# Performance work log

Measured on AMD Instinct MI355X. Metric: run time of the kernel, lower is better.

The kernel has to match this reference:

```python
import jax, jax.numpy as jnp
import numpy as np

HEADS = 8
DIM_HEAD = 64
SCALE = DIM_HEAD ** -0.5


def setup_inputs() -> dict:
    key = jax.random.key(0)
    ks = jax.random.split(key, 7)
    B, Nq, Nc = 4, 2048, 2048
    Dq, Dc = 1024, 768
    inner = HEADS * DIM_HEAD  # 512
    x = jax.random.normal(ks[0], (B, Nq, Dq), dtype=jnp.float32)
    context = jax.random.normal(ks[1], (B, Nc, Dc), dtype=jnp.float32)
    # Linear weights stored as (in, out) so y = x @ W, matching torch Linear math.
    Wq = jax.random.normal(ks[2], (Dq, inner), dtype=jnp.float32) * (Dq ** -0.5)
    Wk = jax.random.normal(ks[3], (Dc, inner), dtype=jnp.float32) * (Dc ** -0.5)
    Wv = jax.random.normal(ks[4], (Dc, inner), dtype=jnp.float32) * (Dc ** -0.5)
    Wo = jax.random.normal(ks[5], (inner, Dq), dtype=jnp.float32) * (inner ** -0.5)
    bo = jax.random.normal(ks[6], (Dq,), dtype=jnp.float32) * 0.01
    return {"x": x, "context": context, "Wq": Wq, "Wk": Wk, "Wv": Wv, "Wo": Wo, "bo": bo}


def reference(x, context, Wq, Wk, Wv, Wo, bo):
    B, Nq, _ = x.shape
    # projections -> [b, n, h, d]
    q = (x @ Wq).reshape(B, Nq, HEADS, DIM_HEAD)
    k = (context @ Wk).reshape(B, context.shape[1], HEADS, DIM_HEAD)
    v = (context @ Wv).reshape(B, context.shape[1], HEADS, DIM_HEAD)
    # scores [b, h, i, j]
    sim = jnp.einsum('bihd,bjhd->bhij', q, k) * SCALE
    attn = jax.nn.softmax(sim, axis=-1)
    out = jnp.einsum('bhij,bjhd->bihd', attn, v)  # [b, i, h, d]
    out = out.reshape(B, Nq, HEADS * DIM_HEAD)
    return out @ Wo + bo
```

## Files before the change

### kernel.cpp

```cpp
#include <hip/hip_runtime.h>
#include <hip/hip_bf16.h>


typedef __bf16 bf16_8 __attribute__((ext_vector_type(8)));
typedef __bf16 bf16_4 __attribute__((ext_vector_type(4)));
typedef float f32_4 __attribute__((ext_vector_type(4)));

#define AS1 __attribute__((address_space(1)))
#define AS3 __attribute__((address_space(3)))

__device__ __forceinline__ void gld_lds16(const __bf16* g, __bf16* l) {
  __builtin_amdgcn_global_load_lds((AS1 unsigned int*)(void*)g,
                                   (AS3 unsigned int*)(void*)l, 16, 0, 0);
}

__device__ __forceinline__ void lds_fence() {
  __asm__ volatile("" ::: "memory");
  __builtin_amdgcn_s_waitcnt(0xC07F);
  __asm__ volatile("" ::: "memory");
}

__global__ __launch_bounds__(256) void prep(
    const float* __restrict__ x, const float* __restrict__ ctx,
    const float* __restrict__ Wq, const float* __restrict__ Wk,
    const float* __restrict__ Wv, const float* __restrict__ Wo,
    __bf16* __restrict__ xb, __bf16* __restrict__ ctxb,
    __bf16* __restrict__ WqT, __bf16* __restrict__ WkT,
    __bf16* __restrict__ WvT, __bf16* __restrict__ WoT) {
  int tb = blockIdx.x;
  if (tb >= 1792) {
    tb -= 1792;
    const float* src;
    __bf16* dst;
    size_t base;
    if (tb < 4096) { src = x; dst = xb; base = (size_t)tb * 2048; }
    else { src = ctx; dst = ctxb; base = (size_t)(tb - 4096) * 2048; }
    const size_t idx = base + threadIdx.x * 8;
    const f32_4 f0 = *(const f32_4*)(src + idx);
    const f32_4 f1 = *(const f32_4*)(src + idx + 4);
    bf16_8 v;
#pragma unroll
    for (int i = 0; i < 4; ++i) { v[i] = (__bf16)f0[i]; v[4 + i] = (__bf16)f1[i]; }
    *(bf16_8*)(dst + idx) = v;
    return;
  }
  __shared__ __bf16 t[32][33];
  const float* W; __bf16* Wt; int K, N;
  if (tb < 512)       { W = Wq; Wt = WqT; K = 1024; N = 512; }
  else if (tb < 896)  { tb -= 512;  W = Wk; Wt = WkT; K = 768; N = 512; }
  else if (tb < 1280) { tb -= 896;  W = Wv; Wt = WvT; K = 768; N = 512; }
  else                { tb -= 1280; W = Wo; Wt = WoT; K = 512; N = 1024; }
  const int nx = N >> 5;
  const int n0 = (tb % nx) * 32, k0 = (tb / nx) * 32;
  const int tx = threadIdx.x & 31, ty = threadIdx.x >> 5;
#pragma unroll
  for (int r = 0; r < 32; r += 8)
    t[ty + r][tx] = (__bf16)W[(size_t)(k0 + ty + r) * N + n0 + tx];
  __syncthreads();
#pragma unroll
  for (int r = 0; r < 32; r += 8)
    Wt[(size_t)(n0 + ty + r) * K + k0 + tx] = t[tx][ty + r];
}

__global__ __launch_bounds__(256, 2) void proj(
    const __bf16* __restrict__ xb, const __bf16* __restrict__ ctxb,
    const __bf16* __restrict__ WqT, const __bf16* __restrict__ WkvT,
    __bf16* __restrict__ Qb, __bf16* __restrict__ Kbuf,
    __bf16* __restrict__ Vtb) {
  __shared__ __align__(16) __bf16 As[2][128 * 64];
  __shared__ __align__(16) __bf16 Bs[2][128 * 64];
  int tb = blockIdx.x;
  const __bf16 *A, *Bt;
  int K, bm, bn, mode;
  if (tb < 256) {
    A = xb; Bt = WqT; K = 1024; mode = 0;
    bn = (tb & 3) << 7; bm = (tb >> 2) << 7;
  } else {
    tb -= 256;
    A = ctxb; Bt = WkvT; K = 768; mode = 1;
    bn = (tb & 7) << 7; bm = (tb >> 3) << 7;
  }
  const int tid = threadIdx.x;
  const int lane = tid & 63;
  const int wave = tid >> 6;
  const int wi = (wave >> 1) * 64;
  const int wn = (wave & 1) * 64;
  const int lrow = lane & 15;
  const int quad = lane >> 4;
  const int lkey = lrow & 7;
  const int srow = tid >> 3;
  const int scol = (tid & 7) * 8;
  const int swz = (((scol >> 3) ^ (srow & 7)) * 8);

  f32_4 acc[4][4];
#pragma unroll
  for (int i = 0; i < 4; ++i)
#pragma unroll
    for (int j = 0; j < 4; ++j)
#pragma unroll
      for (int r = 0; r < 4; ++r) acc[i][j][r] = 0.0f;

  auto stage = [&](int buf, int kt) {
#pragma unroll
    for (int r = 0; r < 4; ++r) {
      const int row = r * 32 + srow;
      gld_lds16(A + (size_t)(bm + row) * K + kt + swz, &As[buf][row * 64 + scol]);
    }
#pragma unroll
    for (int r = 0; r < 4; ++r) {
      const int row = r * 32 + srow;
      gld_lds16(Bt + (size_t)(bn + row) * K + kt + swz, &Bs[buf][row * 64 + scol]);
    }
  };

  stage(0, 0);
  const int nkt = K >> 6;
  for (int kti = 0; kti < nkt; ++kti) {
    __syncthreads();
    if (kti + 1 < nkt) stage((kti + 1) & 1, (kti + 1) * 64);
    const __bf16* Asb = As[kti & 1];
    const __bf16* Bsb = Bs[kti & 1];
#pragma unroll
    for (int ks = 0; ks < 2; ++ks) {
      bf16_8 af[4], bfv[4];
#pragma unroll
      for (int t = 0; t < 4; ++t)
        af[t] = *(const bf16_8*)(Asb + (wi + t * 16 + lrow) * 64 +
                                 (((ks * 4 + quad) ^ lkey) * 8));
#pragma unroll
      for (int t = 0; t < 4; ++t)
        bfv[t] = *(const bf16_8*)(Bsb + (wn + t * 16 + lrow) * 64 +
                                  (((ks * 4 + quad) ^ lkey) * 8));
#pragma unroll
      for (int it = 0; it < 4; ++it)
#pragma unroll
        for (int nt = 0; nt < 4; ++nt)
          acc[it][nt] = __builtin_amdgcn_mfma_f32_16x16x32_bf16(
              af[it], bfv[nt], acc[it][nt], 0, 0, 0);
    }
  }

#pragma unroll
  for (int nt = 0; nt < 4; ++nt) {
    const int c = bn + wn + nt * 16 + lrow;
    if (mode == 0) {
#pragma unroll
      for (int it = 0; it < 4; ++it) {
        const int rbase = bm + wi + it * 16 + quad * 4;
#pragma unroll
        for (int r = 0; r < 4; ++r)
          Qb[(size_t)(rbase + r) * 512 + c] = (__bf16)(acc[it][nt][r] * 0.125f);
      }
    } else if (c < 512) {
#pragma unroll
      for (int it = 0; it < 4; ++it) {
        const int rbase = bm + wi + it * 16 + quad * 4;
#pragma unroll
        for (int r = 0; r < 4; ++r)
          Kbuf[(size_t)(rbase + r) * 512 + c] = (__bf16)acc[it][nt][r];
      }
    } else {
      const int vcol = c - 512;
      const int bhh = ((bm >> 11) << 3) + (vcol >> 6);
      const int d = vcol & 63;
#pragma unroll
      for (int it = 0; it < 4; ++it) {
        const int jb = (bm & 2047) + wi + it * 16 + quad * 4;
        bf16_4 pk;
#pragma unroll
        for (int r = 0; r < 4; ++r) pk[r] = (__bf16)acc[it][nt][r];
        *(bf16_4*)&Vtb[((size_t)(bhh * 64 + d)) * 2048 + jb] = pk;
      }
    }
  }
}

__global__ __launch_bounds__(256, 4) void attn_fwd(const __bf16* __restrict__ Q,
                                                   const __bf16* __restrict__ Kb,
                                                   const __bf16* __restrict__ Vt,
                                                   __bf16* __restrict__ AO) {
  __shared__ __align__(16) __bf16 Ks[2][64 * 64];
  __shared__ __align__(16) __bf16 Vs[2][64 * 64];
  __shared__ __align__(16) __bf16 Pl[4][16 * 64];
  const int tid = threadIdx.x;
  const int lane = tid & 63;
  const int wave = tid >> 6;
  const int did = blockIdx.x;
  const int sid = did >> 3;
  const int bh = ((did & 7) << 2) + (sid & 3);
  const int ib = sid >> 2;
  const int b = bh >> 3, h = bh & 7;
  const int i0 = ib * 64 + wave * 16;
  const int lrow = lane & 15;
  const int quad = lane >> 4;
  const int lkey = lrow & 7;
  const size_t bq = (size_t)b * 2048;
  const int hc = h * 64;
  __bf16* Pw = &Pl[wave][0];

  const int ssub = lane >> 3;
  const int sch = lane & 7;
  const int sswz = (sch ^ ssub) * 8;

  const __bf16* Kg = Kb + bq * 512 + hc;
  const __bf16* Vg = Vt + (size_t)bh * 64 * 2048;

  auto stage = [&](int buf, int j0) {
#pragma unroll
    for (int t = 0; t < 2; ++t) {
      const int rb = wave * 16 + t * 8;
      gld_lds16(Kg + (size_t)(j0 + rb + ssub) * 512 + sswz, &Ks[buf][rb * 64]);
      gld_lds16(Vg + (size_t)(rb + ssub) * 2048 + j0 + sswz, &Vs[buf][rb * 64]);
    }
  };

  bf16_8 aq[2];
#pragma unroll
  for (int ks = 0; ks < 2; ++ks)
    aq[ks] = *(const bf16_8*)(Q + (bq + i0 + lrow) * 512 +
                              hc + ks * 32 + quad * 8);

  float psl = 0.0f;
  f32_4 oacc[4];
#pragma unroll
  for (int nt = 0; nt < 4; ++nt)
#pragma unroll
    for (int r = 0; r < 4; ++r) oacc[nt][r] = 0.0f;

  stage(0, 0);

  for (int jt = 0; jt < 32; ++jt) {
    __syncthreads();
    if (jt + 1 < 32) stage((jt + 1) & 1, (jt + 1) * 64);
    const __bf16* Ksb = Ks[jt & 1];
    const __bf16* Vsb = Vs[jt & 1];

    f32_4 sacc[4];
#pragma unroll
    for (int jn = 0; jn < 4; ++jn)
#pragma unroll
      for (int r = 0; r < 4; ++r) sacc[jn][r] = 0.0f;
    __builtin_amdgcn_s_setprio(1);
#pragma unroll
    for (int ks = 0; ks < 2; ++ks) {
      bf16_8 ak[4];
#pragma unroll
      for (int jn = 0; jn < 4; ++jn)
        ak[jn] = *(const bf16_8*)(Ksb + (jn * 16 + lrow) * 64 +
                                  (((ks * 4 + quad) ^ lkey) * 8));
#pragma unroll
      for (int jn = 0; jn < 4; ++jn)
        sacc[jn] = __builtin_amdgcn_mfma_f32_16x16x32_bf16(
            ak[jn], aq[ks], sacc[jn], 0, 0, 0);
    }
    __builtin_amdgcn_s_setprio(0);

    {
      float ps = 0.0f;
#pragma unroll
      for (int jn = 0; jn < 4; ++jn) {
        bf16_4 pk;
#pragma unroll
        for (int r = 0; r < 4; ++r) {
          const float p = __expf(sacc[jn][r]);
          ps += p;
          pk[r] = (__bf16)p;
        }
        *(bf16_4*)(Pw + lrow * 64 +
                   (((2 * jn + (quad >> 1)) ^ lkey) * 8) + (quad & 1) * 4) = pk;
      }
      psl += ps;
    }

    lds_fence();

    __builtin_amdgcn_s_setprio(1);
#pragma unroll
    for (int ks2 = 0; ks2 < 2; ++ks2) {
      bf16_8 ap, bv[4];
      ap = *(const bf16_8*)(Pw + lrow * 64 + (((ks2 * 4 + quad) ^ lkey) * 8));
#pragma unroll
      for (int nt = 0; nt < 4; ++nt)
        bv[nt] = *(const bf16_8*)(Vsb + (nt * 16 + lrow) * 64 +
                                  (((ks2 * 4 + quad) ^ lkey) * 8));
#pragma unroll
      for (int nt = 0; nt < 4; ++nt)
        oacc[nt] = __builtin_amdgcn_mfma_f32_16x16x32_bf16(
            ap, bv[nt], oacc[nt], 0, 0, 0);
    }
    __builtin_amdgcn_s_setprio(0);
  }

  {
    float ls = psl;
    ls += __shfl_xor(ls, 16);
    ls += __shfl_xor(ls, 32);
    const float inv = 1.0f / ls;
    float ic[4];
#pragma unroll
    for (int r = 0; r < 4; ++r) ic[r] = __shfl(inv, quad * 4 + r);
#pragma unroll
    for (int nt = 0; nt < 4; ++nt)
#pragma unroll
      for (int r = 0; r < 4; ++r) {
        const size_t rg = bq + i0 + quad * 4 + r;
        AO[rg * 512 + hc + nt * 16 + lrow] = (__bf16)(oacc[nt][r] * ic[r]);
      }
  }
}

__global__ __launch_bounds__(256, 2) void gemm_out(const __bf16* __restrict__ A,
                                                   const __bf16* __restrict__ Bt,
                                                   float* __restrict__ C,
                                                   const float* __restrict__ bias) {
  __shared__ __align__(16) __bf16 As[2][128 * 64];
  __shared__ __align__(16) __bf16 Bs[2][128 * 64];
  const int K = 512, N = 1024;
  const int tid = threadIdx.x;
  const int lane = tid & 63;
  const int wave = tid >> 6;
  const int wi = (wave >> 1) * 64;
  const int wn = (wave & 1) * 64;
  const int bm = blockIdx.y * 128;
  const int bn = blockIdx.x * 128;
  const int lrow = lane & 15;
  const int quad = lane >> 4;
  const int lkey = lrow & 7;
  const int srow = tid >> 3;
  const int scol = (tid & 7) * 8;
  const int swz = (((scol >> 3) ^ (srow & 7)) * 8);

  f32_4 acc[4][4];
#pragma unroll
  for (int i = 0; i < 4; ++i)
#pragma unroll
    for (int j = 0; j < 4; ++j)
#pragma unroll
      for (int r = 0; r < 4; ++r) acc[i][j][r] = 0.0f;

  auto stage = [&](int buf, int kt) {
#pragma unroll
    for (int r = 0; r < 4; ++r) {
      const int row = r * 32 + srow;
      gld_lds16(A + (size_t)(bm + row) * K + kt + swz, &As[buf][row * 64 + scol]);
      gld_lds16(Bt + (size_t)(bn + row) * K + kt + swz, &Bs[buf][row * 64 + scol]);
    }
  };

  stage(0, 0);
  for (int kti = 0; kti < 8; ++kti) {
    __syncthreads();
    if (kti + 1 < 8) stage((kti + 1) & 1, (kti + 1) * 64);
    const __bf16* Asb = As[kti & 1];
    const __bf16* Bsb = Bs[kti & 1];
#pragma unroll
    for (int ks = 0; ks < 2; ++ks) {
      bf16_8 af[4], bfv[4];
#pragma unroll
      for (int t = 0; t < 4; ++t)
        af[t] = *(const bf16_8*)(Asb + (wi + t * 16 + lrow) * 64 +
                                 (((ks * 4 + quad) ^ lkey) * 8));
#pragma unroll
      for (int t = 0; t < 4; ++t)
        bfv[t] = *(const bf16_8*)(Bsb + (wn + t * 16 + lrow) * 64 +
                                  (((ks * 4 + quad) ^ lkey) * 8));
#pragma unroll
      for (int it = 0; it < 4; ++it)
#pragma unroll
        for (int nt = 0; nt < 4; ++nt)
          acc[it][nt] = __builtin_amdgcn_mfma_f32_16x16x32_bf16(
              af[it], bfv[nt], acc[it][nt], 0, 0, 0);
    }
  }

#pragma unroll
  for (int nt = 0; nt < 4; ++nt) {
    const int c = bn + wn + nt * 16 + lrow;
    const float bv = bias[c];
#pragma unroll
    for (int it = 0; it < 4; ++it) {
      const int rbase = bm + wi + it * 16 + quad * 4;
#pragma unroll
      for (int r = 0; r < 4; ++r)
        C[(size_t)(rbase + r) * N + c] = acc[it][nt][r] + bv;
    }
  }
}

extern "C" void kernel_launch(void* const* d_in, const int* in_sizes, int n_in,
                              void* d_out, int out_size, void* d_ws, size_t ws_size,
                              hipStream_t stream) {
  (void)in_sizes; (void)n_in; (void)out_size; (void)ws_size;
  const float* x   = (const float*)d_in[0];
  const float* ctx = (const float*)d_in[1];
  const float* Wq  = (const float*)d_in[2];
  const float* Wk  = (const float*)d_in[3];
  const float* Wv  = (const float*)d_in[4];
  const float* Wo  = (const float*)d_in[5];
  const float* bo  = (const float*)d_in[6];

  __bf16* ws = (__bf16*)d_ws;
  __bf16* WqT  = ws;
  __bf16* WkT  = WqT + 512 * 1024;
  __bf16* WvT  = WkT + 512 * 768;
  __bf16* WoT  = WvT + 512 * 768;
  __bf16* Qb   = WoT + 1024 * 512;
  __bf16* Kbuf = Qb + 8192 * 512;
  __bf16* Vtb  = Kbuf + 8192 * 512;
  __bf16* AOb  = Vtb + 8192 * 512;
  __bf16* xb   = AOb + 8192 * 512;
  __bf16* ctxb = xb + 8192 * 1024;

  prep<<<8960, 256, 0, stream>>>(x, ctx, Wq, Wk, Wv, Wo,
                                 xb, ctxb, WqT, WkT, WvT, WoT);

  proj<<<768, 256, 0, stream>>>(xb, ctxb, WqT, WkT, Qb, Kbuf, Vtb);

  attn_fwd<<<1024, 256, 0, stream>>>(Qb, Kbuf, Vtb, AOb);

  gemm_out<<<dim3(8, 64), 256, 0, stream>>>(AOb, WoT, (float*)d_out, bo);
}
```

Measured before the change: 221.1 us.

## Switch attention to 32x32x16 MFMA with register-resident P via permlane32 swap

Rewrites the attention kernel to use 32x32x16 bf16 MFMA tiles, with each wave now handling 32 query rows and each block 128 rows, which halves the grid. The exponentiated scores are packed with v_cvt_pk_bf16_f32 and rearranged across lanes with permlane32_swap, so P goes straight into the PV MFMA operand instead of round-tripping through LDS. This removes the per-tile LDS write, fence and read of P, and halves K/V staging per query row. In exchange it uses more registers (launch bounds drop to 3 blocks per SM) and launches fewer blocks, so there is less parallelism to hide latency.

```diff
diff --git a/kernel.cpp b/kernel.cpp
--- a/kernel.cpp
+++ b/kernel.cpp
@@ -5,6 +5,9 @@
 typedef __bf16 bf16_8 __attribute__((ext_vector_type(8)));
 typedef __bf16 bf16_4 __attribute__((ext_vector_type(4)));
 typedef float f32_4 __attribute__((ext_vector_type(4)));
+typedef float f32_16 __attribute__((ext_vector_type(16)));
+typedef int i32x2 __attribute__((ext_vector_type(2)));
+typedef int i32x4 __attribute__((ext_vector_type(4)));
 
 #define AS1 __attribute__((address_space(1)))
 #define AS3 __attribute__((address_space(3)))
@@ -18,6 +21,12 @@
   __asm__ volatile("" ::: "memory");
   __builtin_amdgcn_s_waitcnt(0xC07F);
   __asm__ volatile("" ::: "memory");
+}
+
+__device__ __forceinline__ int cvt_pk(float lo, float hi) {
+  int r;
+  __asm__("v_cvt_pk_bf16_f32 %0, %1, %2" : "=v"(r) : "v"(lo), "v"(hi));
+  return r;
 }
 
 __global__ __launch_bounds__(256) void prep(
@@ -175,13 +184,13 @@
   }
 }
 
-__global__ __launch_bounds__(256, 4) void attn_fwd(const __bf16* __restrict__ Q,
+__global__ __launch_bounds__(256, 3) void attn_fwd(const __bf16* __restrict__ Q,
                                                    const __bf16* __restrict__ Kb,
                                                    const __bf16* __restrict__ Vt,
                                                    __bf16* __restrict__ AO) {
   __shared__ __align__(16) __bf16 Ks[2][64 * 64];
   __shared__ __align__(16) __bf16 Vs[2][64 * 64];
-  __shared__ __align__(16) __bf16 Pl[4][16 * 64];
+  __shared__ __align__(16) float Ls[4][32];
   const int tid = threadIdx.x;
   const int lane = tid & 63;
   const int wave = tid >> 6;
@@ -190,13 +199,12 @@
   const int bh = ((did & 7) << 2) + (sid & 3);
   const int ib = sid >> 2;
   const int b = bh >> 3, h = bh & 7;
-  const int i0 = ib * 64 + wave * 16;
-  const int lrow = lane & 15;
-  const int quad = lane >> 4;
-  const int lkey = lrow & 7;
+  const int i0 = ib * 128 + wave * 32;
+  const int li = lane & 31;
+  const int hi = lane >> 5;
+  const int key = li & 7;
   const size_t bq = (size_t)b * 2048;
   const int hc = h * 64;
-  __bf16* Pw = &Pl[wave][0];
 
   const int ssub = lane >> 3;
   const int sch = lane & 7;
@@ -214,18 +222,17 @@
     }
   };
 
-  bf16_8 aq[2];
-#pragma unroll
-  for (int ks = 0; ks < 2; ++ks)
-    aq[ks] = *(const bf16_8*)(Q + (bq + i0 + lrow) * 512 +
-                              hc + ks * 32 + quad * 8);
+  bf16_8 aq[4];
+#pragma unroll
+  for (int ks = 0; ks < 4; ++ks)
+    aq[ks] = *(const bf16_8*)(Q + (bq + i0 + li) * 512 + hc + ks * 16 + hi * 8);
 
   float psl = 0.0f;
-  f32_4 oacc[4];
-#pragma unroll
-  for (int nt = 0; nt < 4; ++nt)
-#pragma unroll
-    for (int r = 0; r < 4; ++r) oacc[nt][r] = 0.0f;
+  f32_16 oacc[2];
+#pragma unroll
+  for (int d = 0; d < 2; ++d)
+#pragma unroll
+    for (int r = 0; r < 16; ++r) oacc[d][r] = 0.0f;
 
   stage(0, 0);
 
@@ -235,78 +242,85 @@
     const __bf16* Ksb = Ks[jt & 1];
     const __bf16* Vsb = Vs[jt & 1];
 
-    f32_4 sacc[4];
-#pragma unroll
-    for (int jn = 0; jn < 4; ++jn)
-#pragma unroll
-      for (int r = 0; r < 4; ++r) sacc[jn][r] = 0.0f;
+    f32_16 sacc[2];
+#pragma unroll
+    for (int jb = 0; jb < 2; ++jb)
+#pragma unroll
+      for (int r = 0; r < 16; ++r) sacc[jb][r] = 0.0f;
     __builtin_amdgcn_s_setprio(1);
 #pragma unroll
-    for (int ks = 0; ks < 2; ++ks) {
-      bf16_8 ak[4];
-#pragma unroll
-      for (int jn = 0; jn < 4; ++jn)
-        ak[jn] = *(const bf16_8*)(Ksb + (jn * 16 + lrow) * 64 +
-                                  (((ks * 4 + quad) ^ lkey) * 8));
-#pragma unroll
-      for (int jn = 0; jn < 4; ++jn)
-        sacc[jn] = __builtin_amdgcn_mfma_f32_16x16x32_bf16(
-            ak[jn], aq[ks], sacc[jn], 0, 0, 0);
+    for (int jb = 0; jb < 2; ++jb) {
+#pragma unroll
+      for (int ks = 0; ks < 4; ++ks) {
+        const bf16_8 ak = *(const bf16_8*)(
+            Ksb + (jb * 32 + li) * 64 + (((ks * 2 + hi) ^ key) * 8));
+        sacc[jb] = __builtin_amdgcn_mfma_f32_32x32x16_bf16(
+            ak, aq[ks], sacc[jb], 0, 0, 0);
+      }
     }
     __builtin_amdgcn_s_setprio(0);
 
-    {
-      float ps = 0.0f;
-#pragma unroll
-      for (int jn = 0; jn < 4; ++jn) {
-        bf16_4 pk;
-#pragma unroll
-        for (int r = 0; r < 4; ++r) {
-          const float p = __expf(sacc[jn][r]);
-          ps += p;
-          pk[r] = (__bf16)p;
-        }
-        *(bf16_4*)(Pw + lrow * 64 +
-                   (((2 * jn + (quad >> 1)) ^ lkey) * 8) + (quad & 1) * 4) = pk;
-      }
-      psl += ps;
-    }
-
-    lds_fence();
+    int pw[4][4];
+#pragma unroll
+    for (int jb = 0; jb < 2; ++jb) {
+      float p[16];
+#pragma unroll
+      for (int r = 0; r < 16; ++r) p[r] = __expf(sacc[jb][r]);
+      float s0 = 0.0f, s1 = 0.0f;
+#pragma unroll
+      for (int r = 0; r < 8; ++r) { s0 += p[2 * r]; s1 += p[2 * r + 1]; }
+      psl += s0 + s1;
+      const int c01 = cvt_pk(p[0], p[1]),   c23 = cvt_pk(p[2], p[3]);
+      const int c45 = cvt_pk(p[4], p[5]),   c67 = cvt_pk(p[6], p[7]);
+      const int c89 = cvt_pk(p[8], p[9]),   cab = cvt_pk(p[10], p[11]);
+      const int ccd = cvt_pk(p[12], p[13]), cef = cvt_pk(p[14], p[15]);
+      const i32x2 r02 = __builtin_amdgcn_permlane32_swap(c01, c45, false, false);
+      const i32x2 r13 = __builtin_amdgcn_permlane32_swap(c23, c67, false, false);
+      const i32x2 r46 = __builtin_amdgcn_permlane32_swap(c89, ccd, false, false);
+      const i32x2 r57 = __builtin_amdgcn_permlane32_swap(cab, cef, false, false);
+      pw[jb * 2][0] = r02[0];     pw[jb * 2][1] = r13[0];
+      pw[jb * 2][2] = r02[1];     pw[jb * 2][3] = r13[1];
+      pw[jb * 2 + 1][0] = r46[0]; pw[jb * 2 + 1][1] = r57[0];
+      pw[jb * 2 + 1][2] = r46[1]; pw[jb * 2 + 1][3] = r57[1];
+    }
 
     __builtin_amdgcn_s_setprio(1);
 #pragma unroll
-    for (int ks2 = 0; ks2 < 2; ++ks2) {
-      bf16_8 ap, bv[4];
-      ap = *(const bf16_8*)(Pw + lrow * 64 + (((ks2 * 4 + quad) ^ lkey) * 8));
-#pragma unroll
-      for (int nt = 0; nt < 4; ++nt)
-        bv[nt] = *(const bf16_8*)(Vsb + (nt * 16 + lrow) * 64 +
-                                  (((ks2 * 4 + quad) ^ lkey) * 8));
-#pragma unroll
-      for (int nt = 0; nt < 4; ++nt)
-        oacc[nt] = __builtin_amdgcn_mfma_f32_16x16x32_bf16(
-            ap, bv[nt], oacc[nt], 0, 0, 0);
+    for (int ks2 = 0; ks2 < 4; ++ks2) {
+      i32x4 w4;
+      w4[0] = pw[ks2][0]; w4[1] = pw[ks2][1];
+      w4[2] = pw[ks2][2]; w4[3] = pw[ks2][3];
+      const bf16_8 ap = __builtin_bit_cast(bf16_8, w4);
+#pragma unroll
+      for (int dblk = 0; dblk < 2; ++dblk) {
+        const bf16_8 bv = *(const bf16_8*)(
+            Vsb + (dblk * 32 + li) * 64 + (((ks2 * 2 + hi) ^ key) * 8));
+        oacc[dblk] = __builtin_amdgcn_mfma_f32_32x32x16_bf16(
+            ap, bv, oacc[dblk], 0, 0, 0);
+      }
     }
     __builtin_amdgcn_s_setprio(0);
   }
 
-  {
-    float ls = psl;
-    ls += __shfl_xor(ls, 16);
-    ls += __shfl_xor(ls, 32);
-    const float inv = 1.0f / ls;
-    float ic[4];
-#pragma unroll
-    for (int r = 0; r < 4; ++r) ic[r] = __shfl(inv, quad * 4 + r);
-#pragma unroll
-    for (int nt = 0; nt < 4; ++nt)
+  const float tot = psl + __shfl_xor(psl, 32);
+  const float inv = 1.0f / tot;
+  if (lane < 32) Ls[wave][li] = inv;
+  lds_fence();
+  f32_4 ic[4];
+#pragma unroll
+  for (int g = 0; g < 4; ++g)
+    ic[g] = *(const f32_4*)(&Ls[wave][8 * g + 4 * hi]);
+
+#pragma unroll
+  for (int dblk = 0; dblk < 2; ++dblk)
+#pragma unroll
+    for (int g = 0; g < 4; ++g)
 #pragma unroll
       for (int r = 0; r < 4; ++r) {
-        const size_t rg = bq + i0 + quad * 4 + r;
-        AO[rg * 512 + hc + nt * 16 + lrow] = (__bf16)(oacc[nt][r] * ic[r]);
-      }
-  }
+        const size_t rg = bq + i0 + 8 * g + 4 * hi + r;
+        AO[rg * 512 + hc + dblk * 32 + li] =
+            (__bf16)(oacc[dblk][4 * g + r] * ic[g][r]);
+      }
 }
 
 __global__ __launch_bounds__(256, 2) void gemm_out(const __bf16* __restrict__ A,
@@ -416,7 +430,7 @@
 
   proj<<<768, 256, 0, stream>>>(xb, ctxb, WqT, WkT, Qb, Kbuf, Vtb);
 
-  attn_fwd<<<1024, 256, 0, stream>>>(Qb, Kbuf, Vtb, AOb);
+  attn_fwd<<<512, 256, 0, stream>>>(Qb, Kbuf, Vtb, AOb);
 
   gemm_out<<<dim3(8, 64), 256, 0, stream>>>(AOb, WoT, (float*)d_out, bo);
 }
```

Measured after the change: 217.3 us. Within noise of the previous version (-1.7%).
